# Performance work log

Hardware: AMD Instinct MI355X
Metric: run time of the kernel (lower is better)

## Reference

```python
import jax, jax.numpy as jnp
import numpy as np

NUM_HEADS = 16
KEY_DIM = 64
NUM_FEATURES = 256
D_MODEL = NUM_HEADS * KEY_DIM
EPS = 1e-6


def softmax_kernel(data, proj):
    # data: [..., N, D], proj: [D, F]
    # Faithful to source: ratio uses proj.shape[0] (=D), matching the TF code.
    data_normalizer = 1.0 / jnp.sqrt(jnp.sqrt(jnp.asarray(data.shape[-1], data.dtype)))
    ratio = 1.0 / jnp.sqrt(jnp.asarray(proj.shape[0], data.dtype))
    data = data_normalizer * data
    data_dash = jnp.einsum('...nd,df->...nf', data, proj)
    diag = jnp.sum(jnp.square(data), axis=-1, keepdims=True)  # [..., N, 1]
    return ratio * (jnp.exp(data_dash - diag / 2.0) + EPS)


def setup_inputs() -> dict:
    key = jax.random.key(0)
    ks = jax.random.split(key, 12)
    B, N = 4, 4096
    s = 1.0 / np.sqrt(D_MODEL)
    inp = {
        'queries': jax.random.normal(ks[0], (B, N, D_MODEL), jnp.float32),
        'keys': jax.random.normal(ks[1], (B, N, D_MODEL), jnp.float32),
        'Wq': jax.random.normal(ks[2], (D_MODEL, D_MODEL), jnp.float32) * s,
        'bq': jnp.zeros((D_MODEL,), jnp.float32),
        'Wk': jax.random.normal(ks[3], (D_MODEL, D_MODEL), jnp.float32) * s,
        'bk': jnp.zeros((D_MODEL,), jnp.float32),
        'Wv': jax.random.normal(ks[4], (D_MODEL, D_MODEL), jnp.float32) * s,
        'bv': jnp.zeros((D_MODEL,), jnp.float32),
        'Wo': jax.random.normal(ks[5], (D_MODEL, D_MODEL), jnp.float32) * s,
        'bo': jnp.zeros((D_MODEL,), jnp.float32),
        # GlorotNormal for [KEY_DIM, NUM_FEATURES]
        'proj': jax.random.normal(ks[6], (KEY_DIM, NUM_FEATURES), jnp.float32)
                * np.sqrt(2.0 / (KEY_DIM + NUM_FEATURES)),
    }
    return inp


def reference(queries, keys, Wq, bq, Wk, bk, Wv, bv, Wo, bo, proj):
    # Original code uses x = queries for q, k, v (self-attention); keys arg unused.
    x = queries
    B, N, _ = x.shape
    H, D = NUM_HEADS, KEY_DIM

    def split_heads(t):
        return t.reshape(B, N, H, D).transpose(0, 2, 1, 3)  # [B,H,N,D]

    q = split_heads(x @ Wq + bq)
    k = split_heads(x @ Wk + bk)
    v = split_heads(x @ Wv + bv)

    q_prime = softmax_kernel(q, proj)  # [B,H,N,F]
    k_prime = softmax_kernel(k, proj)  # [B,H,N,F]

    kv = jnp.einsum('bhnf,bhnd->bhfd', k_prime, v)        # [B,H,F,D]
    qkv = jnp.einsum('bhnf,bhfd->bhnd', q_prime, kv)       # [B,H,N,D]
    k_sum = jnp.sum(k_prime, axis=2)                        # [B,H,F]
    norm = jnp.einsum('bhnf,bhf->bhn', q_prime, k_sum) + EPS
    qkv = qkv / norm[..., None]

    out = qkv.transpose(0, 2, 1, 3).reshape(B, N, H * D)    # [B,N,d_model]
    return out @ Wo + bo
```

## Files before the change

### kernel.cpp

```cpp
#include <hip/hip_runtime.h>

typedef __attribute__((ext_vector_type(8))) short short8;
typedef __attribute__((ext_vector_type(4))) float f32x4;

#define MFMA16 __builtin_amdgcn_mfma_f32_16x16x32_bf16

#define GLOAD16(gp, lp) __builtin_amdgcn_global_load_lds(                      \
    (const __attribute__((address_space(1))) void*)(gp),                       \
    (__attribute__((address_space(3))) void*)(lp), 16, 0, 0)

__device__ __forceinline__ unsigned short f2bf(float f) {
  unsigned int u = __float_as_uint(f);
  unsigned int r = u + 0x7fffu + ((u >> 16) & 1u);
  return (unsigned short)(r >> 16);
}
__device__ __forceinline__ float bf2f(unsigned short h) {
  return __uint_as_float(((unsigned int)h) << 16);
}

__global__ __launch_bounds__(256) void cast_x_kernel(
    const float* __restrict__ in, unsigned short* __restrict__ out, int n4) {
  int i = blockIdx.x * 256 + threadIdx.x;
  if (i >= n4) return;
  float4 v = reinterpret_cast<const float4*>(in)[i];
  ushort4 o;
  o.x = f2bf(v.x); o.y = f2bf(v.y); o.z = f2bf(v.z); o.w = f2bf(v.w);
  reinterpret_cast<ushort4*>(out)[i] = o;
}

__global__ __launch_bounds__(256) void tcast_f32_kernel(
    const float* __restrict__ in, unsigned short* __restrict__ out, int R, int C) {
  __shared__ float t[64][65];
  int c0 = blockIdx.x * 64, r0 = blockIdx.y * 64;
  int tx = threadIdx.x, ty = threadIdx.y;
#pragma unroll
  for (int i = 0; i < 16; ++i)
    t[ty + 4 * i][tx] = in[(size_t)(r0 + ty + 4 * i) * C + c0 + tx];
  __syncthreads();
#pragma unroll
  for (int i = 0; i < 16; ++i)
    out[(size_t)(c0 + ty + 4 * i) * R + r0 + tx] = f2bf(t[tx][ty + 4 * i]);
}

__global__ __launch_bounds__(256) void t_bf16_kernel(
    const unsigned short* __restrict__ in, unsigned short* __restrict__ out, int R, int C) {
  __shared__ unsigned short t[64][66];
  size_t base = (size_t)blockIdx.z * (size_t)R * (size_t)C;
  int c0 = blockIdx.x * 64, r0 = blockIdx.y * 64;
  int tx = threadIdx.x, ty = threadIdx.y;
#pragma unroll
  for (int i = 0; i < 16; ++i)
    t[ty + 4 * i][tx] = in[base + (size_t)(r0 + ty + 4 * i) * C + c0 + tx];
  __syncthreads();
#pragma unroll
  for (int i = 0; i < 16; ++i)
    out[base + (size_t)(c0 + ty + 4 * i) * R + r0 + tx] = t[tx][ty + 4 * i];
}

template <int OUTF>
__global__ __launch_bounds__(256) void gemm_bt_kernel(
    const unsigned short* __restrict__ A,
    const unsigned short* W0, const unsigned short* W1, const unsigned short* W2,
    const float* b0, const float* b1, const float* b2,
    void* o0, void* o1, void* o2) {
  constexpr int KD = 1024, ND = 1024;
  const unsigned short* W = W0; const float* bias = b0; void* op = o0;
  if (blockIdx.z == 1) { W = W1; bias = b1; op = o1; }
  else if (blockIdx.z == 2) { W = W2; bias = b2; op = o2; }

  __shared__ unsigned short lsA[128 * 32];
  __shared__ unsigned short lsB[128 * 32];
  int tid = threadIdx.x;
  int w = tid >> 6, lane = tid & 63;
  int m0 = blockIdx.x * 128, n0 = blockIdx.y * 128;
  int wm = (w >> 1) * 64, wn = (w & 1) * 64;

  int srow0 = (w * 2 + 0) * 16 + (lane >> 2);
  int srow1 = (w * 2 + 1) * 16 + (lane >> 2);
  int scol = (lane & 3) * 8;
  const unsigned short* gA0 = A + (size_t)(m0 + srow0) * KD + scol;
  const unsigned short* gA1 = A + (size_t)(m0 + srow1) * KD + scol;
  const unsigned short* gB0 = W + (size_t)(n0 + srow0) * KD + scol;
  const unsigned short* gB1 = W + (size_t)(n0 + srow1) * KD + scol;
  unsigned short* lA0 = &lsA[(w * 2 + 0) * 512];
  unsigned short* lA1 = &lsA[(w * 2 + 1) * 512];
  unsigned short* lB0 = &lsB[(w * 2 + 0) * 512];
  unsigned short* lB1 = &lsB[(w * 2 + 1) * 512];

  f32x4 acc[4][4];
#pragma unroll
  for (int fm = 0; fm < 4; ++fm)
#pragma unroll
    for (int fn = 0; fn < 4; ++fn) acc[fm][fn] = (f32x4){0.f, 0.f, 0.f, 0.f};

  for (int kt = 0; kt < KD; kt += 32) {
    GLOAD16(gA0 + kt, lA0);
    GLOAD16(gA1 + kt, lA1);
    GLOAD16(gB0 + kt, lB0);
    GLOAD16(gB1 + kt, lB1);
    __syncthreads();
    short8 af[4], bfr[4];
#pragma unroll
    for (int fm = 0; fm < 4; ++fm)
      af[fm] = *reinterpret_cast<const short8*>(
          &lsA[(wm + fm * 16 + (lane & 15)) * 32 + (lane >> 4) * 8]);
#pragma unroll
    for (int fn = 0; fn < 4; ++fn)
      bfr[fn] = *reinterpret_cast<const short8*>(
          &lsB[(wn + fn * 16 + (lane & 15)) * 32 + (lane >> 4) * 8]);
#pragma unroll
    for (int fm = 0; fm < 4; ++fm)
#pragma unroll
      for (int fn = 0; fn < 4; ++fn)
        acc[fm][fn] = MFMA16(af[fm], bfr[fn], acc[fm][fn], 0, 0, 0);
    __syncthreads();
  }

#pragma unroll
  for (int fn = 0; fn < 4; ++fn) {
    int col = n0 + wn + fn * 16 + (lane & 15);
    float bv = bias[col];
#pragma unroll
    for (int fm = 0; fm < 4; ++fm) {
#pragma unroll
      for (int j = 0; j < 4; ++j) {
        int row = m0 + wm + fm * 16 + (lane >> 4) * 4 + j;
        float v = acc[fm][fn][j] + bv;
        if (OUTF)
          reinterpret_cast<float*>(op)[(size_t)row * ND + col] = v;
        else
          reinterpret_cast<unsigned short*>(op)[(size_t)row * ND + col] = f2bf(v);
      }
    }
  }
}

__global__ __launch_bounds__(256) void kv_fused_kernel(
    const unsigned short* __restrict__ K, const unsigned short* __restrict__ PT,
    const unsigned short* __restrict__ VT,
    float* __restrict__ kvp, float* __restrict__ ksp) {
  __shared__ unsigned short kp[256 * 40];
  int s = blockIdx.x, bh = blockIdx.y, b = bh >> 4, h = bh & 15;
  int tid = threadIdx.x, w = tid >> 6, lane = tid & 63;
  int lo = lane & 15, hi = lane >> 4;
  int f0w = w * 64;

  short8 pb[4][2];
#pragma unroll
  for (int fn = 0; fn < 4; ++fn) {
    int f = f0w + fn * 16 + lo;
    pb[fn][0] = *reinterpret_cast<const short8*>(PT + (size_t)f * 64 + hi * 8);
    pb[fn][1] = *reinterpret_cast<const short8*>(PT + (size_t)f * 64 + 32 + hi * 8);
  }
  const unsigned short* vbase[4];
#pragma unroll
  for (int fn = 0; fn < 4; ++fn)
    vbase[fn] = VT + (size_t)(bh * 64 + fn * 16 + lo) * 4096;

  f32x4 acck[4][4];
#pragma unroll
  for (int fm = 0; fm < 4; ++fm)
#pragma unroll
    for (int fn = 0; fn < 4; ++fn) acck[fm][fn] = (f32x4){0.f, 0.f, 0.f, 0.f};
  float ks[4] = {0.f, 0.f, 0.f, 0.f};

  for (int c = 0; c < 16; ++c) {
    int n0 = s * 512 + c * 32;
    const unsigned short* Ab = K + (size_t)(b * 4096 + n0) * 1024 + h * 64;
    short8 af[2][2];
    float dp[2] = {0.f, 0.f};
#pragma unroll
    for (int fm = 0; fm < 2; ++fm)
#pragma unroll
      for (int kt = 0; kt < 2; ++kt) {
        af[fm][kt] = *reinterpret_cast<const short8*>(
            Ab + (size_t)(fm * 16 + lo) * 1024 + kt * 32 + hi * 8);
#pragma unroll
        for (int j = 0; j < 8; ++j) {
          float qv = bf2f((unsigned short)af[fm][kt][j]);
          dp[fm] += qv * qv;
        }
      }
#pragma unroll
    for (int fm = 0; fm < 2; ++fm) {
      dp[fm] += __shfl_xor(dp[fm], 16);
      dp[fm] += __shfl_xor(dp[fm], 32);
    }
    f32x4 accf[2][4];
#pragma unroll
    for (int fm = 0; fm < 2; ++fm)
#pragma unroll
      for (int fn = 0; fn < 4; ++fn) accf[fm][fn] = (f32x4){0.f, 0.f, 0.f, 0.f};
#pragma unroll
    for (int fn = 0; fn < 4; ++fn) {
      accf[0][fn] = MFMA16(af[0][0], pb[fn][0], accf[0][fn], 0, 0, 0);
      accf[0][fn] = MFMA16(af[0][1], pb[fn][1], accf[0][fn], 0, 0, 0);
      accf[1][fn] = MFMA16(af[1][0], pb[fn][0], accf[1][fn], 0, 0, 0);
      accf[1][fn] = MFMA16(af[1][1], pb[fn][1], accf[1][fn], 0, 0, 0);
    }
#pragma unroll
    for (int fm = 0; fm < 2; ++fm)
#pragma unroll
      for (int fn = 0; fn < 4; ++fn)
#pragma unroll
        for (int j = 0; j < 4; ++j) {
          float dg = __shfl(dp[fm], hi * 4 + j);
          float v = 0.125f *
                    (__expf(0.35355339059327373f * accf[fm][fn][j] - 0.0625f * dg) + 1e-6f);
          ks[fn] += v;
          kp[(f0w + fn * 16 + lo) * 40 + fm * 16 + hi * 4 + j] = f2bf(v);
        }
    short8 a2[4], b2[4];
#pragma unroll
    for (int fm = 0; fm < 4; ++fm)
      a2[fm] = *reinterpret_cast<const short8*>(&kp[(f0w + fm * 16 + lo) * 40 + hi * 8]);
#pragma unroll
    for (int fn = 0; fn < 4; ++fn)
      b2[fn] = *reinterpret_cast<const short8*>(vbase[fn] + n0 + hi * 8);
#pragma unroll
    for (int fm = 0; fm < 4; ++fm)
#pragma unroll
      for (int fn = 0; fn < 4; ++fn)
        acck[fm][fn] = MFMA16(a2[fm], b2[fn], acck[fm][fn], 0, 0, 0);
  }
#pragma unroll
  for (int fn = 0; fn < 4; ++fn) {
    float v = ks[fn];
    v += __shfl_xor(v, 16);
    v += __shfl_xor(v, 32);
    if (hi == 0)
      ksp[(size_t)(s * 64 + bh) * 256 + f0w + fn * 16 + lo] = v;
  }
#pragma unroll
  for (int fm = 0; fm < 4; ++fm)
#pragma unroll
    for (int fn = 0; fn < 4; ++fn)
#pragma unroll
      for (int j = 0; j < 4; ++j)
        kvp[((size_t)(s * 64 + bh) * 256 + f0w + fm * 16 + hi * 4 + j) * 64 + fn * 16 + lo] =
            acck[fm][fn][j];
}

__global__ __launch_bounds__(256) void kvred_kernel(
    const float* __restrict__ kvp, const float* __restrict__ ksp,
    unsigned short* __restrict__ kvT, float* __restrict__ ksum) {
  int bh = blockIdx.x, tid = threadIdx.x;
  for (int i = tid; i < 64 * 256; i += 256) {
    int f = i >> 6, d = i & 63;
    float sum = 0.f;
#pragma unroll
    for (int s = 0; s < 8; ++s)
      sum += kvp[((size_t)(s * 64 + bh) * 256 + f) * 64 + d];
    kvT[(size_t)(bh * 64 + d) * 256 + f] = f2bf(sum);
  }
  {
    float t = 0.f;
#pragma unroll
    for (int s = 0; s < 8; ++s) t += ksp[(size_t)(s * 64 + bh) * 256 + tid];
    ksum[bh * 256 + tid] = t;
  }
}

__global__ __launch_bounds__(256) void qkv_fused_kernel(
    const unsigned short* __restrict__ Q, const unsigned short* __restrict__ PT,
    const unsigned short* __restrict__ KVT, const float* __restrict__ KSUM,
    unsigned short* __restrict__ Y) {
  __shared__ unsigned short qp[128 * 256];
  int bh = blockIdx.y, b = bh >> 4, h = bh & 15;
  int t0 = blockIdx.x * 128;
  int tid = threadIdx.x, w = tid >> 6, lane = tid & 63;
  int lo = lane & 15, hi = lane >> 4;
  int r0 = w * 32;
  const unsigned short* Ab = Q + (size_t)(b * 4096 + t0 + r0) * 1024 + h * 64;

  float ksr[16];
#pragma unroll
  for (int fn = 0; fn < 16; ++fn) ksr[fn] = KSUM[bh * 256 + fn * 16 + lo];

  short8 af[2][2];
  float dp[2] = {0.f, 0.f};
#pragma unroll
  for (int fm = 0; fm < 2; ++fm)
#pragma unroll
    for (int kt = 0; kt < 2; ++kt) {
      af[fm][kt] = *reinterpret_cast<const short8*>(
          Ab + (size_t)(fm * 16 + lo) * 1024 + kt * 32 + hi * 8);
#pragma unroll
      for (int j = 0; j < 8; ++j) {
        float qv = bf2f((unsigned short)af[fm][kt][j]);
        dp[fm] += qv * qv;
      }
    }
#pragma unroll
  for (int fm = 0; fm < 2; ++fm) {
    dp[fm] += __shfl_xor(dp[fm], 16);
    dp[fm] += __shfl_xor(dp[fm], 32);
  }

  float np[2][4] = {{0.f, 0.f, 0.f, 0.f}, {0.f, 0.f, 0.f, 0.f}};
#pragma unroll
  for (int hf = 0; hf < 2; ++hf) {
    f32x4 accf[2][8];
#pragma unroll
    for (int fm = 0; fm < 2; ++fm)
#pragma unroll
      for (int fn = 0; fn < 8; ++fn) accf[fm][fn] = (f32x4){0.f, 0.f, 0.f, 0.f};
#pragma unroll
    for (int fn = 0; fn < 8; ++fn) {
      int f = (hf * 8 + fn) * 16 + lo;
      short8 pb0 = *reinterpret_cast<const short8*>(PT + (size_t)f * 64 + hi * 8);
      short8 pb1 = *reinterpret_cast<const short8*>(PT + (size_t)f * 64 + 32 + hi * 8);
      accf[0][fn] = MFMA16(af[0][0], pb0, accf[0][fn], 0, 0, 0);
      accf[0][fn] = MFMA16(af[0][1], pb1, accf[0][fn], 0, 0, 0);
      accf[1][fn] = MFMA16(af[1][0], pb0, accf[1][fn], 0, 0, 0);
      accf[1][fn] = MFMA16(af[1][1], pb1, accf[1][fn], 0, 0, 0);
    }
#pragma unroll
    for (int fm = 0; fm < 2; ++fm)
#pragma unroll
      for (int fn = 0; fn < 8; ++fn)
#pragma unroll
        for (int j = 0; j < 4; ++j) {
          float dg = __shfl(dp[fm], hi * 4 + j);
          float v = 0.125f *
                    (__expf(0.35355339059327373f * accf[fm][fn][j] - 0.0625f * dg) + 1e-6f);
          np[fm][j] += v * ksr[hf * 8 + fn];
          int row = r0 + fm * 16 + hi * 4 + j;
          int f = (hf * 8 + fn) * 16 + lo;
          int byt = (row * 512 + f * 2) ^ ((row & 7) << 4);
          *reinterpret_cast<unsigned short*>(reinterpret_cast<char*>(qp) + byt) = f2bf(v);
        }
  }
#pragma unroll
  for (int fm = 0; fm < 2; ++fm)
#pragma unroll
    for (int j = 0; j < 4; ++j) {
      np[fm][j] += __shfl_xor(np[fm][j], 1);
      np[fm][j] += __shfl_xor(np[fm][j], 2);
      np[fm][j] += __shfl_xor(np[fm][j], 4);
      np[fm][j] += __shfl_xor(np[fm][j], 8);
    }
  f32x4 acco[2][4];
#pragma unroll
  for (int fm = 0; fm < 2; ++fm)
#pragma unroll
    for (int fn = 0; fn < 4; ++fn) acco[fm][fn] = (f32x4){0.f, 0.f, 0.f, 0.f};
#pragma unroll
  for (int kt2 = 0; kt2 < 8; ++kt2) {
    short8 a2[2], b2[4];
#pragma unroll
    for (int fm = 0; fm < 2; ++fm) {
      int row = r0 + fm * 16 + lo;
      int byt = (row * 512 + kt2 * 64 + hi * 16) ^ ((row & 7) << 4);
      a2[fm] = *reinterpret_cast<const short8*>(reinterpret_cast<char*>(qp) + byt);
    }
#pragma unroll
    for (int fn = 0; fn < 4; ++fn)
      b2[fn] = *reinterpret_cast<const short8*>(
          KVT + (size_t)(bh * 64 + fn * 16 + lo) * 256 + kt2 * 32 + hi * 8);
#pragma unroll
    for (int fm = 0; fm < 2; ++fm)
#pragma unroll
      for (int fn = 0; fn < 4; ++fn)
        acco[fm][fn] = MFMA16(a2[fm], b2[fn], acco[fm][fn], 0, 0, 0);
  }
#pragma unroll
  for (int fm = 0; fm < 2; ++fm)
#pragma unroll
    for (int j = 0; j < 4; ++j) {
      float nv = np[fm][j] + 1e-6f;
      int row = b * 4096 + t0 + r0 + fm * 16 + hi * 4 + j;
#pragma unroll
      for (int fn = 0; fn < 4; ++fn)
        Y[(size_t)row * 1024 + h * 64 + fn * 16 + lo] = f2bf(acco[fm][fn][j] / nv);
    }
}

extern "C" void kernel_launch(void* const* d_in, const int* in_sizes, int n_in,
                              void* d_out, int out_size, void* d_ws, size_t ws_size,
                              hipStream_t stream) {
  (void)in_sizes; (void)n_in; (void)out_size; (void)ws_size;
  const float* x    = (const float*)d_in[0];
  const float* Wq   = (const float*)d_in[2];
  const float* bq   = (const float*)d_in[3];
  const float* Wk   = (const float*)d_in[4];
  const float* bk   = (const float*)d_in[5];
  const float* Wv   = (const float*)d_in[6];
  const float* bv   = (const float*)d_in[7];
  const float* Wo   = (const float*)d_in[8];
  const float* bo   = (const float*)d_in[9];
  const float* proj = (const float*)d_in[10];
  float* out = (float*)d_out;

  constexpr size_t SZ_XB = (size_t)16384 * 1024 * 2;
  constexpr size_t SZ_W  = (size_t)1024 * 1024 * 2;
  constexpr size_t SZ_PT = (size_t)256 * 64 * 2;

  char* p = (char*)d_ws;
  size_t off = 0;
  char* a_xb  = p + off; off += SZ_XB;
  char* a_WqT = p + off; off += SZ_W;
  char* a_WkT = p + off; off += SZ_W;
  char* a_WvT = p + off; off += SZ_W;
  char* a_WoT = p + off; off += SZ_W;
  char* a_pT  = p + off; off += SZ_PT;
  char* a_qb  = p + off; off += SZ_XB;
  char* a_kb  = p + off; off += SZ_XB;
  char* a_ksp  = p + off; off += (size_t)8 * 64 * 256 * 4;
  char* a_kvT  = p + off; off += (size_t)64 * 64 * 256 * 2;
  char* a_ksum = p + off; off += (size_t)64 * 256 * 4;

  char* a_kvp = a_xb;
  char* a_y = a_kb;
  char* a_vb = (char*)d_out;
  char* a_vT = (char*)d_out + SZ_XB;

  dim3 tb(64, 4);

  cast_x_kernel<<<16384, 256, 0, stream>>>(x, (unsigned short*)a_xb, 16384 * 1024 / 4);
  tcast_f32_kernel<<<dim3(16, 16), tb, 0, stream>>>(Wq, (unsigned short*)a_WqT, 1024, 1024);
  tcast_f32_kernel<<<dim3(16, 16), tb, 0, stream>>>(Wk, (unsigned short*)a_WkT, 1024, 1024);
  tcast_f32_kernel<<<dim3(16, 16), tb, 0, stream>>>(Wv, (unsigned short*)a_WvT, 1024, 1024);
  tcast_f32_kernel<<<dim3(16, 16), tb, 0, stream>>>(Wo, (unsigned short*)a_WoT, 1024, 1024);
  tcast_f32_kernel<<<dim3(4, 1), tb, 0, stream>>>(proj, (unsigned short*)a_pT, 64, 256);

  gemm_bt_kernel<0><<<dim3(128, 8, 3), 256, 0, stream>>>(
      (unsigned short*)a_xb,
      (unsigned short*)a_WqT, (unsigned short*)a_WkT, (unsigned short*)a_WvT,
      bq, bk, bv, a_qb, a_kb, a_vb);

  t_bf16_kernel<<<dim3(16, 64, 4), tb, 0, stream>>>(
      (unsigned short*)a_vb, (unsigned short*)a_vT, 4096, 1024);

  kv_fused_kernel<<<dim3(8, 64), 256, 0, stream>>>(
      (unsigned short*)a_kb, (unsigned short*)a_pT, (unsigned short*)a_vT,
      (float*)a_kvp, (float*)a_ksp);
  kvred_kernel<<<64, 256, 0, stream>>>(
      (float*)a_kvp, (float*)a_ksp, (unsigned short*)a_kvT, (float*)a_ksum);

  qkv_fused_kernel<<<dim3(32, 64), 256, 0, stream>>>(
      (unsigned short*)a_qb, (unsigned short*)a_pT, (unsigned short*)a_kvT,
      (float*)a_ksum, (unsigned short*)a_y);

  gemm_bt_kernel<1><<<dim3(128, 8, 1), 256, 0, stream>>>(
      (unsigned short*)a_y,
      (unsigned short*)a_WoT, nullptr, nullptr,
      bo, nullptr, nullptr, out, nullptr, nullptr);
}
```

Before: 356.4 us.

## Fuse V transpose into GEMM epilogue, split KV reduction finer, interleave qkv stages

The V projection GEMM now writes its output already transposed by staging the tile in dynamic shared memory, which removes the separate bf16 transpose kernel and its round trip through memory. The four weight cast-transposes are merged into one launch. The kv kernel splits the sequence into 16 chunks instead of 8 for more parallelism, and the reduction kernel is spread over a 2-D grid with a shared-memory transpose so kvT is written with vectorized stores. The qkv kernel overlaps the second matmul with each half of the feature computation, which halves its shared-memory buffer and may raise occupancy, at the cost of more partial-result traffic and an extra GEMM launch.

```diff
diff --git a/kernel.cpp b/kernel.cpp
--- a/kernel.cpp
+++ b/kernel.cpp
@@ -42,19 +42,25 @@
     out[(size_t)(c0 + ty + 4 * i) * R + r0 + tx] = f2bf(t[tx][ty + 4 * i]);
 }
 
-__global__ __launch_bounds__(256) void t_bf16_kernel(
-    const unsigned short* __restrict__ in, unsigned short* __restrict__ out, int R, int C) {
-  __shared__ unsigned short t[64][66];
-  size_t base = (size_t)blockIdx.z * (size_t)R * (size_t)C;
+__global__ __launch_bounds__(256) void tcast4_kernel(
+    const float* __restrict__ i0, const float* __restrict__ i1,
+    const float* __restrict__ i2, const float* __restrict__ i3,
+    unsigned short* __restrict__ o0, unsigned short* __restrict__ o1,
+    unsigned short* __restrict__ o2, unsigned short* __restrict__ o3) {
+  const float* in = i0; unsigned short* out = o0;
+  if (blockIdx.z == 1) { in = i1; out = o1; }
+  else if (blockIdx.z == 2) { in = i2; out = o2; }
+  else if (blockIdx.z == 3) { in = i3; out = o3; }
+  __shared__ float t[64][65];
   int c0 = blockIdx.x * 64, r0 = blockIdx.y * 64;
   int tx = threadIdx.x, ty = threadIdx.y;
 #pragma unroll
   for (int i = 0; i < 16; ++i)
-    t[ty + 4 * i][tx] = in[base + (size_t)(r0 + ty + 4 * i) * C + c0 + tx];
+    t[ty + 4 * i][tx] = in[(size_t)(r0 + ty + 4 * i) * 1024 + c0 + tx];
   __syncthreads();
 #pragma unroll
   for (int i = 0; i < 16; ++i)
-    out[base + (size_t)(c0 + ty + 4 * i) * R + r0 + tx] = t[tx][ty + 4 * i];
+    out[(size_t)(c0 + ty + 4 * i) * 1024 + r0 + tx] = f2bf(t[tx][ty + 4 * i]);
 }
 
 template <int OUTF>
@@ -70,6 +76,7 @@
 
   __shared__ unsigned short lsA[128 * 32];
   __shared__ unsigned short lsB[128 * 32];
+  extern __shared__ unsigned short tt[];
   int tid = threadIdx.x;
   int w = tid >> 6, lane = tid & 63;
   int m0 = blockIdx.x * 128, n0 = blockIdx.y * 128;
@@ -118,19 +125,35 @@
 
 #pragma unroll
   for (int fn = 0; fn < 4; ++fn) {
-    int col = n0 + wn + fn * 16 + (lane & 15);
-    float bv = bias[col];
+    int coll = wn + fn * 16 + (lane & 15);
+    float bv = bias[n0 + coll];
 #pragma unroll
     for (int fm = 0; fm < 4; ++fm) {
 #pragma unroll
       for (int j = 0; j < 4; ++j) {
-        int row = m0 + wm + fm * 16 + (lane >> 4) * 4 + j;
+        int rowl = wm + fm * 16 + (lane >> 4) * 4 + j;
         float v = acc[fm][fn][j] + bv;
-        if (OUTF)
-          reinterpret_cast<float*>(op)[(size_t)row * ND + col] = v;
-        else
-          reinterpret_cast<unsigned short*>(op)[(size_t)row * ND + col] = f2bf(v);
+        if constexpr (OUTF == 2) {
+          tt[coll * 136 + rowl] = f2bf(v);
+        } else if constexpr (OUTF == 1) {
+          reinterpret_cast<float*>(op)[(size_t)(m0 + rowl) * ND + n0 + coll] = v;
+        } else {
+          reinterpret_cast<unsigned short*>(op)[(size_t)(m0 + rowl) * ND + n0 + coll] =
+              f2bf(v);
+        }
       }
+    }
+  }
+  if constexpr (OUTF == 2) {
+    __syncthreads();
+    int b = m0 >> 12, tok0 = m0 & 4095;
+    int c = tid >> 1, half = (tid & 1) * 64;
+    unsigned short* dst = reinterpret_cast<unsigned short*>(op) +
+                          (size_t)(b * 1024 + n0 + c) * 4096 + tok0 + half;
+#pragma unroll
+    for (int i = 0; i < 8; ++i) {
+      short8 vv = *reinterpret_cast<const short8*>(&tt[c * 136 + half + i * 8]);
+      *reinterpret_cast<short8*>(dst + i * 8) = vv;
     }
   }
 }
@@ -138,12 +161,14 @@
 __global__ __launch_bounds__(256) void kv_fused_kernel(
     const unsigned short* __restrict__ K, const unsigned short* __restrict__ PT,
     const unsigned short* __restrict__ VT,
-    float* __restrict__ kvp, float* __restrict__ ksp) {
+    float* __restrict__ kvp0, float* __restrict__ kvp1, float* __restrict__ ksp) {
   __shared__ unsigned short kp[256 * 40];
   int s = blockIdx.x, bh = blockIdx.y, b = bh >> 4, h = bh & 15;
   int tid = threadIdx.x, w = tid >> 6, lane = tid & 63;
   int lo = lane & 15, hi = lane >> 4;
   int f0w = w * 64;
+  float* kvp = (s < 8) ? kvp0 : kvp1;
+  int sl = s & 7;
 
   short8 pb[4][2];
 #pragma unroll
@@ -164,8 +189,8 @@
     for (int fn = 0; fn < 4; ++fn) acck[fm][fn] = (f32x4){0.f, 0.f, 0.f, 0.f};
   float ks[4] = {0.f, 0.f, 0.f, 0.f};
 
-  for (int c = 0; c < 16; ++c) {
-    int n0 = s * 512 + c * 32;
+  for (int c = 0; c < 8; ++c) {
+    int n0 = s * 256 + c * 32;
     const unsigned short* Ab = K + (size_t)(b * 4096 + n0) * 1024 + h * 64;
     short8 af[2][2];
     float dp[2] = {0.f, 0.f};
@@ -237,27 +262,43 @@
     for (int fn = 0; fn < 4; ++fn)
 #pragma unroll
       for (int j = 0; j < 4; ++j)
-        kvp[((size_t)(s * 64 + bh) * 256 + f0w + fm * 16 + hi * 4 + j) * 64 + fn * 16 + lo] =
+        kvp[((size_t)(sl * 64 + bh) * 256 + f0w + fm * 16 + hi * 4 + j) * 64 + fn * 16 + lo] =
             acck[fm][fn][j];
 }
 
 __global__ __launch_bounds__(256) void kvred_kernel(
-    const float* __restrict__ kvp, const float* __restrict__ ksp,
+    const float* __restrict__ kvp0, const float* __restrict__ kvp1,
+    const float* __restrict__ ksp,
     unsigned short* __restrict__ kvT, float* __restrict__ ksum) {
-  int bh = blockIdx.x, tid = threadIdx.x;
-  for (int i = tid; i < 64 * 256; i += 256) {
-    int f = i >> 6, d = i & 63;
-    float sum = 0.f;
-#pragma unroll
-    for (int s = 0; s < 8; ++s)
-      sum += kvp[((size_t)(s * 64 + bh) * 256 + f) * 64 + d];
-    kvT[(size_t)(bh * 64 + d) * 256 + f] = f2bf(sum);
-  }
-  {
-    float t = 0.f;
-#pragma unroll
-    for (int s = 0; s < 8; ++s) t += ksp[(size_t)(s * 64 + bh) * 256 + tid];
-    ksum[bh * 256 + tid] = t;
+  __shared__ float t[64][65];
+  int bh = blockIdx.x, g = blockIdx.y, tid = threadIdx.x;
+  int fbase = g * 64;
+  int fo = tid >> 2, dq = (tid & 3) * 16;
+  float sum[16];
+#pragma unroll
+  for (int i = 0; i < 16; ++i) sum[i] = 0.f;
+#pragma unroll
+  for (int s = 0; s < 16; ++s) {
+    const float* base = ((s < 8) ? kvp0 : kvp1) +
+                        ((size_t)((s & 7) * 64 + bh) * 256 + fbase + fo) * 64 + dq;
+#pragma unroll
+    for (int i = 0; i < 16; ++i) sum[i] += base[i];
+  }
+#pragma unroll
+  for (int i = 0; i < 16; ++i) t[fo][dq + i] = sum[i];
+  __syncthreads();
+  int d = tid >> 2, fq = (tid & 3) * 16;
+  unsigned short wv[16];
+#pragma unroll
+  for (int i = 0; i < 16; ++i) wv[i] = f2bf(t[fq + i][d]);
+  unsigned short* dst = kvT + (size_t)(bh * 64 + d) * 256 + fbase + fq;
+  *reinterpret_cast<short8*>(dst) = *reinterpret_cast<const short8*>(&wv[0]);
+  *reinterpret_cast<short8*>(dst + 8) = *reinterpret_cast<const short8*>(&wv[8]);
+  if (g == 0) {
+    float tsum = 0.f;
+#pragma unroll
+    for (int s = 0; s < 16; ++s) tsum += ksp[(size_t)(s * 64 + bh) * 256 + tid];
+    ksum[bh * 256 + tid] = tsum;
   }
 }
 
@@ -265,7 +306,7 @@
     const unsigned short* __restrict__ Q, const unsigned short* __restrict__ PT,
     const unsigned short* __restrict__ KVT, const float* __restrict__ KSUM,
     unsigned short* __restrict__ Y) {
-  __shared__ unsigned short qp[128 * 256];
+  __shared__ unsigned short qp[128 * 128];
   int bh = blockIdx.y, b = bh >> 4, h = bh & 15;
   int t0 = blockIdx.x * 128;
   int tid = threadIdx.x, w = tid >> 6, lane = tid & 63;
@@ -298,6 +339,12 @@
   }
 
   float np[2][4] = {{0.f, 0.f, 0.f, 0.f}, {0.f, 0.f, 0.f, 0.f}};
+  f32x4 acco[2][4];
+#pragma unroll
+  for (int fm = 0; fm < 2; ++fm)
+#pragma unroll
+    for (int fn = 0; fn < 4; ++fn) acco[fm][fn] = (f32x4){0.f, 0.f, 0.f, 0.f};
+
 #pragma unroll
   for (int hf = 0; hf < 2; ++hf) {
     f32x4 accf[2][8];
@@ -307,7 +354,7 @@
       for (int fn = 0; fn < 8; ++fn) accf[fm][fn] = (f32x4){0.f, 0.f, 0.f, 0.f};
 #pragma unroll
     for (int fn = 0; fn < 8; ++fn) {
-      int f = (hf * 8 + fn) * 16 + lo;
+      int f = hf * 128 + fn * 16 + lo;
       short8 pb0 = *reinterpret_cast<const short8*>(PT + (size_t)f * 64 + hi * 8);
       short8 pb1 = *reinterpret_cast<const short8*>(PT + (size_t)f * 64 + 32 + hi * 8);
       accf[0][fn] = MFMA16(af[0][0], pb0, accf[0][fn], 0, 0, 0);
@@ -326,10 +373,29 @@
                     (__expf(0.35355339059327373f * accf[fm][fn][j] - 0.0625f * dg) + 1e-6f);
           np[fm][j] += v * ksr[hf * 8 + fn];
           int row = r0 + fm * 16 + hi * 4 + j;
-          int f = (hf * 8 + fn) * 16 + lo;
-          int byt = (row * 512 + f * 2) ^ ((row & 7) << 4);
+          int fl = fn * 16 + lo;
+          int byt = (row * 256 + fl * 2) ^ ((row & 7) << 4);
           *reinterpret_cast<unsigned short*>(reinterpret_cast<char*>(qp) + byt) = f2bf(v);
         }
+#pragma unroll
+    for (int kt2 = 0; kt2 < 4; ++kt2) {
+      short8 a2[2], b2[4];
+#pragma unroll
+      for (int fm = 0; fm < 2; ++fm) {
+        int row = r0 + fm * 16 + lo;
+        int byt = (row * 256 + kt2 * 64 + hi * 16) ^ ((row & 7) << 4);
+        a2[fm] = *reinterpret_cast<const short8*>(reinterpret_cast<char*>(qp) + byt);
+      }
+#pragma unroll
+      for (int fn = 0; fn < 4; ++fn)
+        b2[fn] = *reinterpret_cast<const short8*>(
+            KVT + (size_t)(bh * 64 + fn * 16 + lo) * 256 + hf * 128 + kt2 * 32 + hi * 8);
+#pragma unroll
+      for (int fm = 0; fm < 2; ++fm)
+#pragma unroll
+        for (int fn = 0; fn < 4; ++fn)
+          acco[fm][fn] = MFMA16(a2[fm], b2[fn], acco[fm][fn], 0, 0, 0);
+    }
   }
 #pragma unroll
   for (int fm = 0; fm < 2; ++fm)
@@ -340,30 +406,6 @@
       np[fm][j] += __shfl_xor(np[fm][j], 4);
       np[fm][j] += __shfl_xor(np[fm][j], 8);
     }
-  f32x4 acco[2][4];
-#pragma unroll
-  for (int fm = 0; fm < 2; ++fm)
-#pragma unroll
-    for (int fn = 0; fn < 4; ++fn) acco[fm][fn] = (f32x4){0.f, 0.f, 0.f, 0.f};
-#pragma unroll
-  for (int kt2 = 0; kt2 < 8; ++kt2) {
-    short8 a2[2], b2[4];
-#pragma unroll
-    for (int fm = 0; fm < 2; ++fm) {
-      int row = r0 + fm * 16 + lo;
-      int byt = (row * 512 + kt2 * 64 + hi * 16) ^ ((row & 7) << 4);
-      a2[fm] = *reinterpret_cast<const short8*>(reinterpret_cast<char*>(qp) + byt);
-    }
-#pragma unroll
-    for (int fn = 0; fn < 4; ++fn)
-      b2[fn] = *reinterpret_cast<const short8*>(
-          KVT + (size_t)(bh * 64 + fn * 16 + lo) * 256 + kt2 * 32 + hi * 8);
-#pragma unroll
-    for (int fm = 0; fm < 2; ++fm)
-#pragma unroll
-      for (int fn = 0; fn < 4; ++fn)
-        acco[fm][fn] = MFMA16(a2[fm], b2[fn], acco[fm][fn], 0, 0, 0);
-  }
 #pragma unroll
   for (int fm = 0; fm < 2; ++fm)
 #pragma unroll
@@ -406,37 +448,39 @@
   char* a_pT  = p + off; off += SZ_PT;
   char* a_qb  = p + off; off += SZ_XB;
   char* a_kb  = p + off; off += SZ_XB;
-  char* a_ksp  = p + off; off += (size_t)8 * 64 * 256 * 4;
+  char* a_ksp  = p + off; off += (size_t)16 * 64 * 256 * 4;
   char* a_kvT  = p + off; off += (size_t)64 * 64 * 256 * 2;
   char* a_ksum = p + off; off += (size_t)64 * 256 * 4;
 
-  char* a_kvp = a_xb;
+  char* a_kvp0 = a_xb;
+  char* a_kvp1 = (char*)d_out + SZ_XB;
+  char* a_vT = (char*)d_out;
   char* a_y = a_kb;
-  char* a_vb = (char*)d_out;
-  char* a_vT = (char*)d_out + SZ_XB;
 
   dim3 tb(64, 4);
 
   cast_x_kernel<<<16384, 256, 0, stream>>>(x, (unsigned short*)a_xb, 16384 * 1024 / 4);
-  tcast_f32_kernel<<<dim3(16, 16), tb, 0, stream>>>(Wq, (unsigned short*)a_WqT, 1024, 1024);
-  tcast_f32_kernel<<<dim3(16, 16), tb, 0, stream>>>(Wk, (unsigned short*)a_WkT, 1024, 1024);
-  tcast_f32_kernel<<<dim3(16, 16), tb, 0, stream>>>(Wv, (unsigned short*)a_WvT, 1024, 1024);
-  tcast_f32_kernel<<<dim3(16, 16), tb, 0, stream>>>(Wo, (unsigned short*)a_WoT, 1024, 1024);
+  tcast4_kernel<<<dim3(16, 16, 4), tb, 0, stream>>>(
+      Wq, Wk, Wv, Wo,
+      (unsigned short*)a_WqT, (unsigned short*)a_WkT,
+      (unsigned short*)a_WvT, (unsigned short*)a_WoT);
   tcast_f32_kernel<<<dim3(4, 1), tb, 0, stream>>>(proj, (unsigned short*)a_pT, 64, 256);
 
-  gemm_bt_kernel<0><<<dim3(128, 8, 3), 256, 0, stream>>>(
+  gemm_bt_kernel<0><<<dim3(128, 8, 2), 256, 0, stream>>>(
       (unsigned short*)a_xb,
-      (unsigned short*)a_WqT, (unsigned short*)a_WkT, (unsigned short*)a_WvT,
-      bq, bk, bv, a_qb, a_kb, a_vb);
-
-  t_bf16_kernel<<<dim3(16, 64, 4), tb, 0, stream>>>(
-      (unsigned short*)a_vb, (unsigned short*)a_vT, 4096, 1024);
-
-  kv_fused_kernel<<<dim3(8, 64), 256, 0, stream>>>(
+      (unsigned short*)a_WqT, (unsigned short*)a_WkT, nullptr,
+      bq, bk, nullptr, a_qb, a_kb, nullptr);
+  gemm_bt_kernel<2><<<dim3(128, 8, 1), 256, 128 * 136 * 2, stream>>>(
+      (unsigned short*)a_xb,
+      (unsigned short*)a_WvT, nullptr, nullptr,
+      bv, nullptr, nullptr, a_vT, nullptr, nullptr);
+
+  kv_fused_kernel<<<dim3(16, 64), 256, 0, stream>>>(
       (unsigned short*)a_kb, (unsigned short*)a_pT, (unsigned short*)a_vT,
-      (float*)a_kvp, (float*)a_ksp);
-  kvred_kernel<<<64, 256, 0, stream>>>(
-      (float*)a_kvp, (float*)a_ksp, (unsigned short*)a_kvT, (float*)a_ksum);
+      (float*)a_kvp0, (float*)a_kvp1, (float*)a_ksp);
+  kvred_kernel<<<dim3(64, 4), 256, 0, stream>>>(
+      (float*)a_kvp0, (float*)a_kvp1, (float*)a_ksp,
+      (unsigned short*)a_kvT, (float*)a_ksum);
 
   qkv_fused_kernel<<<dim3(32, 64), 256, 0, stream>>>(
       (unsigned short*)a_qb, (unsigned short*)a_pT, (unsigned short*)a_kvT,
```

Measured after the change: 373.6 us. 1.05x slower.
